# Kernel optimization log

Measured on AMD Instinct MI355X. Metric: run time of the kernel, lower is better.

Reference implementation:

```python
import jax, jax.numpy as jnp
import numpy as np

D_MODEL = 1024
D_FF = 4096
EPS = 1e-5


def layer_norm(x, gamma, beta):
    mu = jnp.mean(x, axis=-1, keepdims=True)
    var = jnp.var(x, axis=-1, keepdims=True)
    return (x - mu) * jax.lax.rsqrt(var + EPS) * gamma + beta


def attention(x_q, x_kv, WQ, WK, WV, causal):
    Q = x_q @ WQ          # [B,Sq,D]
    K = x_kv @ WK         # [B,Sk,D]
    V = x_kv @ WV
    scale = 1.0 / jnp.sqrt(jnp.asarray(Q.shape[-1], Q.dtype))
    scores = jnp.einsum('bqd,bkd->bqk', Q, K) * scale
    if causal:
        Sq, Sk = scores.shape[-2], scores.shape[-1]
        mask = jnp.triu(jnp.full((Sq, Sk), -jnp.inf, scores.dtype), k=1)
        scores = scores + mask
    attn = jax.nn.softmax(scores, axis=-1)
    return jnp.einsum('bqk,bkd->bqd', attn, V)


def setup_inputs() -> dict:
    key = jax.random.key(0)
    ks = jax.random.split(key, 16)
    B, S = 4, 2048
    s = 0.02
    inp = {
        'y': jax.random.normal(ks[0], (B, S, D_MODEL), jnp.float32),
        'Z': jax.random.normal(ks[1], (B, S, D_MODEL), jnp.float32),
        'WQ1': jax.random.normal(ks[2], (D_MODEL, D_MODEL), jnp.float32) * s,
        'WK1': jax.random.normal(ks[3], (D_MODEL, D_MODEL), jnp.float32) * s,
        'WV1': jax.random.normal(ks[4], (D_MODEL, D_MODEL), jnp.float32) * s,
        'WQ2': jax.random.normal(ks[5], (D_MODEL, D_MODEL), jnp.float32) * s,
        'WK2': jax.random.normal(ks[6], (D_MODEL, D_MODEL), jnp.float32) * s,
        'WV2': jax.random.normal(ks[7], (D_MODEL, D_MODEL), jnp.float32) * s,
        'W_ff1': jax.random.normal(ks[8], (D_MODEL, D_FF), jnp.float32) * s,
        'b_ff1': jnp.zeros((D_FF,), jnp.float32),
        'W_ff2': jax.random.normal(ks[9], (D_FF, D_MODEL), jnp.float32) * s,
        'b_ff2': jnp.zeros((D_MODEL,), jnp.float32),
        'g1': jnp.ones((D_MODEL,), jnp.float32), 'be1': jnp.zeros((D_MODEL,), jnp.float32),
        'g2': jnp.ones((D_MODEL,), jnp.float32), 'be2': jnp.zeros((D_MODEL,), jnp.float32),
        'g3': jnp.ones((D_MODEL,), jnp.float32), 'be3': jnp.zeros((D_MODEL,), jnp.float32),
    }
    return inp


def reference(y, Z, WQ1, WK1, WV1, WQ2, WK2, WV2, W_ff1, b_ff1, W_ff2, b_ff2,
              g1, be1, g2, be2, g3, be3):
    # masked self-attention + add&norm
    y = layer_norm(y + attention(y, y, WQ1, WK1, WV1, causal=True), g1, be1)
    # cross-attention + add&norm
    y = layer_norm(y + attention(y, Z, WQ2, WK2, WV2, causal=False), g2, be2)
    # FFN + add&norm
    h = jax.nn.relu(y @ W_ff1 + b_ff1) @ W_ff2 + b_ff2
    y = layer_norm(y + h, g3, be3)
    return y
```

## Files before the change

### kernel.cpp

```cpp
#include <hip/hip_runtime.h>
#include <cstddef>

typedef unsigned short u16;
typedef __attribute__((ext_vector_type(8))) short bf16x8;
typedef __attribute__((ext_vector_type(4))) float f32x4;

__device__ __forceinline__ u16 f2bf(float f) {
  union { float f; unsigned u; } x; x.f = f;
  unsigned r = x.u + 0x7fffu + ((x.u >> 16) & 1u);
  return (u16)(r >> 16);
}
__device__ __forceinline__ float bf2f(u16 h) {
  union { unsigned u; float f; } x; x.u = ((unsigned)h) << 16;
  return x.f;
}

__device__ __forceinline__ void gll16(const u16* g, u16* ldsbase) {
  __builtin_amdgcn_global_load_lds(
      (const __attribute__((address_space(1))) void*)g,
      (__attribute__((address_space(3))) void*)ldsbase, 16, 0, 0);
}

__global__ __launch_bounds__(256) void f32_to_bf16(const float* __restrict__ in,
                                                   u16* __restrict__ out, size_t n) {
  size_t i = (size_t)blockIdx.x * 256 + threadIdx.x;
  if (i < n) out[i] = f2bf(in[i]);
}

__global__ __launch_bounds__(256) void transpose_f32_bf16(const float* __restrict__ in,
                                                          u16* __restrict__ out,
                                                          int R, int C) {
  __shared__ float tile[32][33];
  int c0 = blockIdx.x * 32, r0 = blockIdx.y * 32;
  int tx = threadIdx.x & 31, ty = threadIdx.x >> 5;
  #pragma unroll
  for (int i = ty; i < 32; i += 8)
    tile[i][tx] = in[(size_t)(r0 + i) * C + c0 + tx];
  __syncthreads();
  #pragma unroll
  for (int i = ty; i < 32; i += 8)
    out[(size_t)(c0 + i) * R + r0 + tx] = f2bf(tile[tx][i]);
}

enum { EPI_F32 = 0, EPI_BF16 = 1, EPI_BF16_SCALE = 2,
       EPI_SPLIT = 3, EPI_BIAS_RELU_BF16 = 4, EPI_BIAS_F32 = 5 };

template <int EPI>
__global__ __launch_bounds__(256) void gemm_bt(
    const u16* __restrict__ A, const u16* __restrict__ Bt,
    void* __restrict__ C0, void* __restrict__ C1, const float* __restrict__ bias,
    int N, int K, int lda, int ldb, int ldc, int split,
    long long sA, long long sB, int sC)
{
  constexpr bool SW = (EPI != EPI_SPLIT);
  __shared__ __align__(16) u16 lA[2][128 * 32];
  __shared__ __align__(16) u16 lB[2][128 * 32];

  const unsigned gx = gridDim.x, gxy = gridDim.x * gridDim.y;
  unsigned id = blockIdx.x + gx * blockIdx.y + gxy * blockIdx.z;
  const unsigned nb = gxy * gridDim.z;
  unsigned p = id;
  if ((nb & 7u) == 0u) p = (id & 7u) * (nb >> 3) + (id >> 3);
  const int z  = p / gxy;
  const unsigned rem = p % gxy;
  const int m0 = (int)(rem / gx) * 128;
  const int n0 = (int)(rem % gx) * 128;

  A  += (long long)z * sA;
  Bt += (long long)z * sB;

  const int t    = threadIdx.x;
  const int lane = t & 63;
  const int wave = t >> 6;
  const int wm   = (wave >> 1) * 64;
  const int wn   = (wave & 1) * 64;
  const int quad = lane >> 4;
  const int lrow = lane & 15;

  const int srow = lane >> 2;
  const int scol = ((lane & 3) ^ ((srow >> 1) & 3)) * 8;
  const u16* gA = A  + (size_t)(m0 + wave * 16 + srow) * lda + scol;
  const u16* gB = Bt + (size_t)(n0 + wave * 16 + srow) * ldb + scol;
  const size_t a64 = (size_t)64 * lda, b64 = (size_t)64 * ldb;
  const int wo = wave * 512;

  const int pq = (quad ^ ((lrow >> 1) & 3)) * 8;

  f32x4 acc[4][4];
  const f32x4 zero = {0.f, 0.f, 0.f, 0.f};
  #pragma unroll
  for (int i = 0; i < 4; i++)
    #pragma unroll
    for (int j = 0; j < 4; j++) acc[i][j] = zero;

  gll16(gA, &lA[0][wo]);
  gll16(gA + a64, &lA[0][wo + 64 * 32]);
  gll16(gB, &lB[0][wo]);
  gll16(gB + b64, &lB[0][wo + 64 * 32]);

  int buf = 0;
  for (int k0 = 0; k0 < K; k0 += 32, buf ^= 1) {
    __syncthreads();
    if (k0 + 32 < K) {
      gll16(gA + k0 + 32, &lA[buf ^ 1][wo]);
      gll16(gA + a64 + k0 + 32, &lA[buf ^ 1][wo + 64 * 32]);
      gll16(gB + k0 + 32, &lB[buf ^ 1][wo]);
      gll16(gB + b64 + k0 + 32, &lB[buf ^ 1][wo + 64 * 32]);
    }

    bf16x8 af[4], bfr[4];
    #pragma unroll
    for (int mt = 0; mt < 4; mt++)
      af[mt] = *(const bf16x8*)(&lA[buf][(wm + mt * 16 + lrow) * 32 + pq]);
    #pragma unroll
    for (int nt = 0; nt < 4; nt++)
      bfr[nt] = *(const bf16x8*)(&lB[buf][(wn + nt * 16 + lrow) * 32 + pq]);

    #pragma unroll
    for (int mt = 0; mt < 4; mt++)
      #pragma unroll
      for (int nt = 0; nt < 4; nt++) {
        if constexpr (SW)
          acc[mt][nt] = __builtin_amdgcn_mfma_f32_16x16x32_bf16(bfr[nt], af[mt], acc[mt][nt], 0, 0, 0);
        else
          acc[mt][nt] = __builtin_amdgcn_mfma_f32_16x16x32_bf16(af[mt], bfr[nt], acc[mt][nt], 0, 0, 0);
      }
  }

  const unsigned zoff = (unsigned)z * (unsigned)sC;
  if constexpr (SW) {
    #pragma unroll
    for (int mt = 0; mt < 4; mt++) {
      #pragma unroll
      for (int nt = 0; nt < 4; nt++) {
        const unsigned m  = (unsigned)(m0 + wm + mt * 16 + lrow);
        const unsigned nc = (unsigned)(n0 + wn + nt * 16 + quad * 4);
        const unsigned idx = zoff + m * (unsigned)ldc + nc;
        f32x4 v = acc[mt][nt];
        if constexpr (EPI == EPI_F32) {
          *(float4*)((float*)C0 + idx) = make_float4(v[0], v[1], v[2], v[3]);
        } else if constexpr (EPI == EPI_BF16) {
          ushort4 o; o.x = f2bf(v[0]); o.y = f2bf(v[1]); o.z = f2bf(v[2]); o.w = f2bf(v[3]);
          *(ushort4*)((u16*)C0 + idx) = o;
        } else if constexpr (EPI == EPI_BF16_SCALE) {
          ushort4 o;
          o.x = f2bf(v[0] * 0.03125f); o.y = f2bf(v[1] * 0.03125f);
          o.z = f2bf(v[2] * 0.03125f); o.w = f2bf(v[3] * 0.03125f);
          *(ushort4*)((u16*)C0 + idx) = o;
        } else if constexpr (EPI == EPI_BIAS_RELU_BF16) {
          const float4 bb = *(const float4*)(bias + nc);
          float y0 = v[0] + bb.x, y1 = v[1] + bb.y, y2 = v[2] + bb.z, y3 = v[3] + bb.w;
          ushort4 o;
          o.x = f2bf(y0 > 0.f ? y0 : 0.f); o.y = f2bf(y1 > 0.f ? y1 : 0.f);
          o.z = f2bf(y2 > 0.f ? y2 : 0.f); o.w = f2bf(y3 > 0.f ? y3 : 0.f);
          *(ushort4*)((u16*)C0 + idx) = o;
        } else {
          const float4 bb = *(const float4*)(bias + nc);
          *(float4*)((float*)C0 + idx) =
              make_float4(v[0] + bb.x, v[1] + bb.y, v[2] + bb.z, v[3] + bb.w);
        }
      }
    }
  } else {
    #pragma unroll
    for (int mt = 0; mt < 4; mt++) {
      #pragma unroll
      for (int nt = 0; nt < 4; nt++) {
        const int row0 = m0 + wm + mt * 16 + quad * 4;
        const int col  = n0 + wn + nt * 16 + lrow;
        if (col < split) {
          const unsigned b0 = (unsigned)row0 * (unsigned)ldc + (unsigned)col;
          #pragma unroll
          for (int r = 0; r < 4; r++)
            ((u16*)C0)[b0 + (unsigned)r * ldc] = f2bf(acc[mt][nt][r]);
        } else {
          const int zp = row0 >> 11;
          const int s  = row0 & 2047;
          const unsigned vo = (unsigned)zp * (unsigned)sC
                            + (unsigned)(col - split) * 2048u + (unsigned)s;
          ushort4 o4;
          o4.x = f2bf(acc[mt][nt][0]); o4.y = f2bf(acc[mt][nt][1]);
          o4.z = f2bf(acc[mt][nt][2]); o4.w = f2bf(acc[mt][nt][3]);
          *(ushort4*)((u16*)C1 + vo) = o4;
        }
      }
    }
  }
}

__global__ __launch_bounds__(256) void softmax_bf16(u16* __restrict__ SP, int causal) {
  __shared__ float red[8];
  const int row = blockIdx.x;
  const int q = row & 2047;
  u16* p = SP + (size_t)row * 2048;
  const int t = threadIdx.x;
  const int base = t * 8;
  const int limit = causal ? (q + 1) : 2048;

  uint4 raw = *(const uint4*)(p + base);
  unsigned w[4] = {raw.x, raw.y, raw.z, raw.w};
  float v[8];
  #pragma unroll
  for (int j = 0; j < 4; j++) {
    union { unsigned u; float f; } lo, hi;
    lo.u = w[j] << 16; hi.u = w[j] & 0xffff0000u;
    v[2 * j] = lo.f; v[2 * j + 1] = hi.f;
  }
  #pragma unroll
  for (int j = 0; j < 8; j++) if (base + j >= limit) v[j] = -3.4e38f;

  float mx = v[0];
  #pragma unroll
  for (int j = 1; j < 8; j++) mx = fmaxf(mx, v[j]);
  #pragma unroll
  for (int o = 32; o > 0; o >>= 1) mx = fmaxf(mx, __shfl_down(mx, o));
  if ((t & 63) == 0) red[t >> 6] = mx;
  __syncthreads();
  mx = fmaxf(fmaxf(red[0], red[1]), fmaxf(red[2], red[3]));

  float s = 0.f;
  #pragma unroll
  for (int j = 0; j < 8; j++) { float e = __expf(v[j] - mx); v[j] = e; s += e; }
  #pragma unroll
  for (int o = 32; o > 0; o >>= 1) s += __shfl_down(s, o);
  if ((t & 63) == 0) red[4 + (t >> 6)] = s;
  __syncthreads();
  const float inv = 1.f / (red[4] + red[5] + red[6] + red[7]);

  unsigned o4[4];
  #pragma unroll
  for (int j = 0; j < 4; j++)
    o4[j] = (unsigned)f2bf(v[2 * j] * inv) | ((unsigned)f2bf(v[2 * j + 1] * inv) << 16);
  *(uint4*)(p + base) = make_uint4(o4[0], o4[1], o4[2], o4[3]);
}

template <int ABF>
__global__ __launch_bounds__(256) void ln_residual(const void* __restrict__ a_,
                                                   const float* __restrict__ b,
                                                   const float* __restrict__ g,
                                                   const float* __restrict__ be,
                                                   float* __restrict__ outf,
                                                   u16* __restrict__ outb) {
  __shared__ float red[8];
  const size_t base = (size_t)blockIdx.x * 1024;
  const int t = threadIdx.x;
  const int i0 = t * 4;

  float va[4];
  if constexpr (ABF) {
    const ushort4 h = *(const ushort4*)((const u16*)a_ + base + i0);
    va[0] = bf2f(h.x); va[1] = bf2f(h.y); va[2] = bf2f(h.z); va[3] = bf2f(h.w);
  } else {
    const float4 f = *(const float4*)((const float*)a_ + base + i0);
    va[0] = f.x; va[1] = f.y; va[2] = f.z; va[3] = f.w;
  }
  const float4 vb = *(const float4*)(b + base + i0);
  float v[4] = {va[0] + vb.x, va[1] + vb.y, va[2] + vb.z, va[3] + vb.w};

  float s = v[0] + v[1] + v[2] + v[3];
  #pragma unroll
  for (int o = 32; o > 0; o >>= 1) s += __shfl_down(s, o);
  if ((t & 63) == 0) red[t >> 6] = s;
  __syncthreads();
  const float mean = (red[0] + red[1] + red[2] + red[3]) * (1.f / 1024.f);

  float qq = 0.f;
  #pragma unroll
  for (int i = 0; i < 4; i++) { float d = v[i] - mean; qq += d * d; }
  #pragma unroll
  for (int o = 32; o > 0; o >>= 1) qq += __shfl_down(qq, o);
  if ((t & 63) == 0) red[4 + (t >> 6)] = qq;
  __syncthreads();
  const float rstd = rsqrtf((red[4] + red[5] + red[6] + red[7]) * (1.f / 1024.f) + 1e-5f);

  const float4 gg = *(const float4*)(g + i0);
  const float4 bb = *(const float4*)(be + i0);
  float y0 = (v[0] - mean) * rstd * gg.x + bb.x;
  float y1 = (v[1] - mean) * rstd * gg.y + bb.y;
  float y2 = (v[2] - mean) * rstd * gg.z + bb.z;
  float y3 = (v[3] - mean) * rstd * gg.w + bb.w;
  if (outf) *(float4*)(outf + base + i0) = make_float4(y0, y1, y2, y3);
  if (outb) {
    ushort4 o4; o4.x = f2bf(y0); o4.y = f2bf(y1); o4.z = f2bf(y2); o4.w = f2bf(y3);
    *(ushort4*)(outb + base + i0) = o4;
  }
}

extern "C" void kernel_launch(void* const* d_in, const int* in_sizes, int n_in,
                              void* d_out, int out_size, void* d_ws, size_t ws_size,
                              hipStream_t stream)
{
  const float* y_in = (const float*)d_in[0];
  const float* Z_in = (const float*)d_in[1];
  const float* WQ1  = (const float*)d_in[2];
  const float* WK1  = (const float*)d_in[3];
  const float* WV1  = (const float*)d_in[4];
  const float* WQ2  = (const float*)d_in[5];
  const float* WK2  = (const float*)d_in[6];
  const float* WV2  = (const float*)d_in[7];
  const float* Wff1 = (const float*)d_in[8];
  const float* bff1 = (const float*)d_in[9];
  const float* Wff2 = (const float*)d_in[10];
  const float* bff2 = (const float*)d_in[11];
  const float* g1  = (const float*)d_in[12];
  const float* be1 = (const float*)d_in[13];
  const float* g2  = (const float*)d_in[14];
  const float* be2 = (const float*)d_in[15];
  const float* g3  = (const float*)d_in[16];
  const float* be3 = (const float*)d_in[17];
  (void)in_sizes; (void)n_in; (void)out_size;

  constexpr int Bn = 4, S = 2048, D = 1024, DF = 4096;
  constexpr long long BS = (long long)Bn * S;
  const long long SD = (long long)S * D, SS = (long long)S * S, DS = (long long)D * S;

  char* ws = (char*)d_ws;
  size_t off = 0;
  auto alloc = [&](size_t bytes) -> char* {
    char* p = ws + off;
    off += (bytes + 255) & ~(size_t)255;
    return p;
  };

  u16* wq1t  = (u16*)alloc((size_t)D * D * 2);
  u16* wk1t  = (u16*)alloc((size_t)D * D * 2);
  u16* wv1t  = (u16*)alloc((size_t)D * D * 2);
  u16* wq2t  = (u16*)alloc((size_t)D * D * 2);
  u16* wk2t  = (u16*)alloc((size_t)D * D * 2);
  u16* wv2t  = (u16*)alloc((size_t)D * D * 2);
  u16* wff1t = (u16*)alloc((size_t)D * DF * 2);
  u16* wff2t = (u16*)alloc((size_t)D * DF * 2);
  u16* ybf   = (u16*)alloc((size_t)BS * D * 2);
  u16* zbf   = (u16*)alloc((size_t)BS * D * 2);
  u16* QKb   = (u16*)alloc((size_t)BS * 2 * D * 2);
  u16* Vtb   = (u16*)alloc((size_t)Bn * D * S * 2);
  u16* SPb   = (u16*)alloc((size_t)Bn * S * S * 2);
  float* attnF = (float*)alloc((size_t)BS * D * 4);
  u16*   y1b = ybf;
  u16*   y2b = zbf;
  u16*   Hb  = QKb;
  float* Fb  = attnF;

  if (off > ws_size) return;

  const dim3 blk(256);

  f32_to_bf16<<<dim3((unsigned)((BS * D) / 256)), blk, 0, stream>>>(y_in, ybf, (size_t)BS * D);
  f32_to_bf16<<<dim3((unsigned)((BS * D) / 256)), blk, 0, stream>>>(Z_in, zbf, (size_t)BS * D);
  transpose_f32_bf16<<<dim3(D / 32, D / 32), blk, 0, stream>>>(WQ1, wq1t, D, D);
  transpose_f32_bf16<<<dim3(D / 32, D / 32), blk, 0, stream>>>(WK1, wk1t, D, D);
  transpose_f32_bf16<<<dim3(D / 32, D / 32), blk, 0, stream>>>(WV1, wv1t, D, D);
  transpose_f32_bf16<<<dim3(D / 32, D / 32), blk, 0, stream>>>(WQ2, wq2t, D, D);
  transpose_f32_bf16<<<dim3(D / 32, D / 32), blk, 0, stream>>>(WK2, wk2t, D, D);
  transpose_f32_bf16<<<dim3(D / 32, D / 32), blk, 0, stream>>>(WV2, wv2t, D, D);
  transpose_f32_bf16<<<dim3(DF / 32, D / 32), blk, 0, stream>>>(Wff1, wff1t, D, DF);
  transpose_f32_bf16<<<dim3(D / 32, DF / 32), blk, 0, stream>>>(Wff2, wff2t, DF, D);

  gemm_bt<EPI_SPLIT><<<dim3(3 * D / 128, BS / 128, 1), blk, 0, stream>>>(
      ybf, wq1t, QKb, Vtb, nullptr, 3 * D, D, D, D, 2 * D, 2 * D, 0, 0, (int)DS);
  gemm_bt<EPI_BF16_SCALE><<<dim3(S / 128, S / 128, Bn), blk, 0, stream>>>(
      QKb, QKb + D, SPb, nullptr, nullptr, S, D, 2 * D, 2 * D, S, 0, SD * 2, SD * 2, (int)SS);
  softmax_bf16<<<dim3((unsigned)(Bn * S)), blk, 0, stream>>>(SPb, 1);
  gemm_bt<EPI_F32><<<dim3(D / 128, S / 128, Bn), blk, 0, stream>>>(
      SPb, Vtb, attnF, nullptr, nullptr, D, S, S, S, D, 0, SS, DS, (int)SD);
  ln_residual<0><<<dim3((unsigned)BS), blk, 0, stream>>>(y_in, attnF, g1, be1, nullptr, y1b);

  gemm_bt<EPI_BF16><<<dim3(D / 128, BS / 128, 1), blk, 0, stream>>>(
      y1b, wq2t, QKb, nullptr, nullptr, D, D, D, D, 2 * D, 0, 0, 0, 0);
  gemm_bt<EPI_SPLIT><<<dim3(2 * D / 128, BS / 128, 1), blk, 0, stream>>>(
      zbf, wk2t, QKb + D, Vtb, nullptr, 2 * D, D, D, D, 2 * D, D, 0, 0, (int)DS);
  gemm_bt<EPI_BF16_SCALE><<<dim3(S / 128, S / 128, Bn), blk, 0, stream>>>(
      QKb, QKb + D, SPb, nullptr, nullptr, S, D, 2 * D, 2 * D, S, 0, SD * 2, SD * 2, (int)SS);
  softmax_bf16<<<dim3((unsigned)(Bn * S)), blk, 0, stream>>>(SPb, 0);
  gemm_bt<EPI_F32><<<dim3(D / 128, S / 128, Bn), blk, 0, stream>>>(
      SPb, Vtb, attnF, nullptr, nullptr, D, S, S, S, D, 0, SS, DS, (int)SD);
  ln_residual<1><<<dim3((unsigned)BS), blk, 0, stream>>>(y1b, attnF, g2, be2, nullptr, y2b);

  gemm_bt<EPI_BIAS_RELU_BF16><<<dim3(DF / 128, BS / 128, 1), blk, 0, stream>>>(
      y2b, wff1t, Hb, nullptr, bff1, DF, D, D, D, DF, 0, 0, 0, 0);
  gemm_bt<EPI_BIAS_F32><<<dim3(D / 128, BS / 128, 1), blk, 0, stream>>>(
      Hb, wff2t, Fb, nullptr, bff2, D, DF, DF, DF, D, 0, 0, 0, 0);
  ln_residual<1><<<dim3((unsigned)BS), blk, 0, stream>>>(y2b, Fb, g3, be3, (float*)d_out, nullptr);
}
```

Baseline: 832.4 us.

## Replace 128x128 GEMM with 256x256 8-wave pipelined kernel and causal skipping

Replaces the 128x128x32 double-buffered GEMM with a 256x256x64 tile kernel using 512 threads. Each k-step is split into four phases that interleave LDS fragment loads, async global-to-LDS staging and MFMA bursts, with raised wave priority around the MFMAs. It also skips masked work in causal self-attention: the QK^T GEMM runs only on lower-triangular tiles, and the PV GEMM stops its K loop at the diagonal. V is now produced as a separate transposed GEMM instead of through the split epilogue. Larger tiles raise LDS use and register pressure and mean fewer blocks per GEMM, and the causal path relies on the softmax writing zeros into the unwritten upper-triangle region.

```diff
diff --git a/kernel.cpp b/kernel.cpp
--- a/kernel.cpp
+++ b/kernel.cpp
@@ -43,146 +43,229 @@
 }
 
 enum { EPI_F32 = 0, EPI_BF16 = 1, EPI_BF16_SCALE = 2,
-       EPI_SPLIT = 3, EPI_BIAS_RELU_BF16 = 4, EPI_BIAS_F32 = 5 };
-
-template <int EPI>
-__global__ __launch_bounds__(256) void gemm_bt(
+       EPI_BIAS_RELU_BF16 = 3, EPI_BIAS_F32 = 4 };
+enum { MODE_FULL = 0, MODE_TRI = 1, MODE_CAUSAL_K = 2 };
+
+template <int EPI, int MODE>
+__global__ __launch_bounds__(512) void gemm256(
     const u16* __restrict__ A, const u16* __restrict__ Bt,
-    void* __restrict__ C0, void* __restrict__ C1, const float* __restrict__ bias,
-    int N, int K, int lda, int ldb, int ldc, int split,
-    long long sA, long long sB, int sC)
+    void* __restrict__ C0, const float* __restrict__ bias,
+    int K, int lda, int ldb, int ldc,
+    long long sA, long long sB, long long sC)
 {
-  constexpr bool SW = (EPI != EPI_SPLIT);
-  __shared__ __align__(16) u16 lA[2][128 * 32];
-  __shared__ __align__(16) u16 lB[2][128 * 32];
+  __shared__ __align__(16) u16 lA[2][256 * 64];
+  __shared__ __align__(16) u16 lB[2][256 * 64];
 
   const unsigned gx = gridDim.x, gxy = gridDim.x * gridDim.y;
   unsigned id = blockIdx.x + gx * blockIdx.y + gxy * blockIdx.z;
   const unsigned nb = gxy * gridDim.z;
   unsigned p = id;
   if ((nb & 7u) == 0u) p = (id & 7u) * (nb >> 3) + (id >> 3);
-  const int z  = p / gxy;
-  const unsigned rem = p % gxy;
-  const int m0 = (int)(rem / gx) * 128;
-  const int n0 = (int)(rem % gx) * 128;
+  int z, mi, ni;
+  if constexpr (MODE == MODE_TRI) {
+    z = (int)(p / gxy);
+    int r = (int)(p % gxy);
+    int m = 0;
+    while ((m + 1) * (m + 2) / 2 <= r) m++;
+    mi = m; ni = r - m * (m + 1) / 2;
+  } else {
+    z = (int)(p / gxy);
+    const unsigned rem = p % gxy;
+    mi = (int)(rem / gx);
+    ni = (int)(rem % gx);
+  }
+  const int m0 = mi * 256, n0 = ni * 256;
 
   A  += (long long)z * sA;
   Bt += (long long)z * sB;
+
+  int NT = K >> 6;
+  if constexpr (MODE == MODE_CAUSAL_K) NT = (m0 + 256) >> 6;
 
   const int t    = threadIdx.x;
   const int lane = t & 63;
   const int wave = t >> 6;
-  const int wm   = (wave >> 1) * 64;
-  const int wn   = (wave & 1) * 64;
+  const int wr   = wave >> 2;
+  const int wc   = wave & 3;
   const int quad = lane >> 4;
   const int lrow = lane & 15;
 
-  const int srow = lane >> 2;
-  const int scol = ((lane & 3) ^ ((srow >> 1) & 3)) * 8;
-  const u16* gA = A  + (size_t)(m0 + wave * 16 + srow) * lda + scol;
-  const u16* gB = Bt + (size_t)(n0 + wave * 16 + srow) * ldb + scol;
+  const int srow = lane >> 3;
+  const int scol = ((lane & 7) ^ srow) * 8;
+  const u16* gAp = A  + (size_t)(m0 + wave * 8 + srow) * lda + scol;
+  const u16* gBp = Bt + (size_t)(n0 + wave * 8 + srow) * ldb + scol;
   const size_t a64 = (size_t)64 * lda, b64 = (size_t)64 * ldb;
-  const int wo = wave * 512;
-
-  const int pq = (quad ^ ((lrow >> 1) & 3)) * 8;
-
-  f32x4 acc[4][4];
+  const int lw = wave * 512;
+
+  const int pg0 = (quad ^ (lrow & 7)) * 8;
+  const int pg1 = pg0 ^ 32;
+  const int rA = (wr * 128 + lrow) * 64;
+  const int rB = (wc * 64 + lrow) * 64;
+
+  f32x4 acc[8][4];
   const f32x4 zero = {0.f, 0.f, 0.f, 0.f};
   #pragma unroll
-  for (int i = 0; i < 4; i++)
+  for (int i = 0; i < 8; i++)
     #pragma unroll
     for (int j = 0; j < 4; j++) acc[i][j] = zero;
 
-  gll16(gA, &lA[0][wo]);
-  gll16(gA + a64, &lA[0][wo + 64 * 32]);
-  gll16(gB, &lB[0][wo]);
-  gll16(gB + b64, &lB[0][wo + 64 * 32]);
-
-  int buf = 0;
-  for (int k0 = 0; k0 < K; k0 += 32, buf ^= 1) {
-    __syncthreads();
-    if (k0 + 32 < K) {
-      gll16(gA + k0 + 32, &lA[buf ^ 1][wo]);
-      gll16(gA + a64 + k0 + 32, &lA[buf ^ 1][wo + 64 * 32]);
-      gll16(gB + k0 + 32, &lB[buf ^ 1][wo]);
-      gll16(gB + b64 + k0 + 32, &lB[buf ^ 1][wo + 64 * 32]);
-    }
-
-    bf16x8 af[4], bfr[4];
-    #pragma unroll
-    for (int mt = 0; mt < 4; mt++)
-      af[mt] = *(const bf16x8*)(&lA[buf][(wm + mt * 16 + lrow) * 32 + pq]);
-    #pragma unroll
-    for (int nt = 0; nt < 4; nt++)
-      bfr[nt] = *(const bf16x8*)(&lB[buf][(wn + nt * 16 + lrow) * 32 + pq]);
-
-    #pragma unroll
-    for (int mt = 0; mt < 4; mt++)
-      #pragma unroll
-      for (int nt = 0; nt < 4; nt++) {
-        if constexpr (SW)
-          acc[mt][nt] = __builtin_amdgcn_mfma_f32_16x16x32_bf16(bfr[nt], af[mt], acc[mt][nt], 0, 0, 0);
-        else
-          acc[mt][nt] = __builtin_amdgcn_mfma_f32_16x16x32_bf16(af[mt], bfr[nt], acc[mt][nt], 0, 0, 0);
-      }
-  }
-
-  const unsigned zoff = (unsigned)z * (unsigned)sC;
-  if constexpr (SW) {
-    #pragma unroll
-    for (int mt = 0; mt < 4; mt++) {
-      #pragma unroll
-      for (int nt = 0; nt < 4; nt++) {
-        const unsigned m  = (unsigned)(m0 + wm + mt * 16 + lrow);
-        const unsigned nc = (unsigned)(n0 + wn + nt * 16 + quad * 4);
-        const unsigned idx = zoff + m * (unsigned)ldc + nc;
-        f32x4 v = acc[mt][nt];
-        if constexpr (EPI == EPI_F32) {
-          *(float4*)((float*)C0 + idx) = make_float4(v[0], v[1], v[2], v[3]);
-        } else if constexpr (EPI == EPI_BF16) {
-          ushort4 o; o.x = f2bf(v[0]); o.y = f2bf(v[1]); o.z = f2bf(v[2]); o.w = f2bf(v[3]);
-          *(ushort4*)((u16*)C0 + idx) = o;
-        } else if constexpr (EPI == EPI_BF16_SCALE) {
-          ushort4 o;
-          o.x = f2bf(v[0] * 0.03125f); o.y = f2bf(v[1] * 0.03125f);
-          o.z = f2bf(v[2] * 0.03125f); o.w = f2bf(v[3] * 0.03125f);
-          *(ushort4*)((u16*)C0 + idx) = o;
-        } else if constexpr (EPI == EPI_BIAS_RELU_BF16) {
-          const float4 bb = *(const float4*)(bias + nc);
-          float y0 = v[0] + bb.x, y1 = v[1] + bb.y, y2 = v[2] + bb.z, y3 = v[3] + bb.w;
-          ushort4 o;
-          o.x = f2bf(y0 > 0.f ? y0 : 0.f); o.y = f2bf(y1 > 0.f ? y1 : 0.f);
-          o.z = f2bf(y2 > 0.f ? y2 : 0.f); o.w = f2bf(y3 > 0.f ? y3 : 0.f);
-          *(ushort4*)((u16*)C0 + idx) = o;
-        } else {
-          const float4 bb = *(const float4*)(bias + nc);
-          *(float4*)((float*)C0 + idx) =
-              make_float4(v[0] + bb.x, v[1] + bb.y, v[2] + bb.z, v[3] + bb.w);
-        }
-      }
-    }
+  auto stage = [&](int b, int s, int kt) {
+    const int k = kt * 64;
+    if (s == 0) {
+      gll16(gBp + k,            &lB[b][lw]);
+      gll16(gBp + k + b64,      &lB[b][4096 + lw]);
+    } else if (s == 1) {
+      gll16(gBp + k + 2 * b64,  &lB[b][8192 + lw]);
+      gll16(gBp + k + 3 * b64,  &lB[b][12288 + lw]);
+    } else if (s == 2) {
+      gll16(gAp + k,            &lA[b][lw]);
+      gll16(gAp + k + a64,      &lA[b][4096 + lw]);
+    } else {
+      gll16(gAp + k + 2 * a64,  &lA[b][8192 + lw]);
+      gll16(gAp + k + 3 * a64,  &lA[b][12288 + lw]);
+    }
+  };
+
+  stage(0, 0, 0); stage(0, 1, 0); stage(0, 2, 0); stage(0, 3, 0);
+  if (NT > 1) {
+    stage(1, 0, 1); stage(1, 1, 1); stage(1, 2, 1);
+    asm volatile("s_waitcnt vmcnt(6)" ::: "memory");
   } else {
-    #pragma unroll
-    for (int mt = 0; mt < 4; mt++) {
-      #pragma unroll
-      for (int nt = 0; nt < 4; nt++) {
-        const int row0 = m0 + wm + mt * 16 + quad * 4;
-        const int col  = n0 + wn + nt * 16 + lrow;
-        if (col < split) {
-          const unsigned b0 = (unsigned)row0 * (unsigned)ldc + (unsigned)col;
-          #pragma unroll
-          for (int r = 0; r < 4; r++)
-            ((u16*)C0)[b0 + (unsigned)r * ldc] = f2bf(acc[mt][nt][r]);
-        } else {
-          const int zp = row0 >> 11;
-          const int s  = row0 & 2047;
-          const unsigned vo = (unsigned)zp * (unsigned)sC
-                            + (unsigned)(col - split) * 2048u + (unsigned)s;
-          ushort4 o4;
-          o4.x = f2bf(acc[mt][nt][0]); o4.y = f2bf(acc[mt][nt][1]);
-          o4.z = f2bf(acc[mt][nt][2]); o4.w = f2bf(acc[mt][nt][3]);
-          *(ushort4*)((u16*)C1 + vo) = o4;
-        }
+    asm volatile("s_waitcnt vmcnt(0)" ::: "memory");
+  }
+  __builtin_amdgcn_s_barrier();
+
+  bf16x8 af[4][2], bfr[4][2];
+
+  for (int kt = 0; kt < NT; ++kt) {
+    const int bsel = kt & 1;
+    const u16* sa = &lA[bsel][0];
+    const u16* sb = &lB[bsel][0];
+
+    #pragma unroll
+    for (int mf = 0; mf < 4; ++mf) {
+      af[mf][0] = *(const bf16x8*)(sa + rA + mf * 1024 + pg0);
+      af[mf][1] = *(const bf16x8*)(sa + rA + mf * 1024 + pg1);
+    }
+    if (wc < 2) {
+      #pragma unroll
+      for (int nf = 0; nf < 4; ++nf) {
+        bfr[nf][0] = *(const bf16x8*)(sb + rB + nf * 1024 + pg0);
+        bfr[nf][1] = *(const bf16x8*)(sb + rB + nf * 1024 + pg1);
+      }
+    } else {
+      #pragma unroll
+      for (int nf = 0; nf < 2; ++nf) {
+        bfr[nf][0] = *(const bf16x8*)(sb + rB + nf * 1024 + pg0);
+        bfr[nf][1] = *(const bf16x8*)(sb + rB + nf * 1024 + pg1);
+      }
+    }
+    if (kt + 1 < NT) stage(bsel ^ 1, 3, kt + 1);
+    __builtin_amdgcn_s_barrier();
+    asm volatile("s_waitcnt lgkmcnt(0)" ::: "memory");
+    __builtin_amdgcn_sched_barrier(0);
+    __builtin_amdgcn_s_setprio(1);
+    #pragma unroll
+    for (int mf = 0; mf < 4; ++mf)
+      #pragma unroll
+      for (int nf = 0; nf < 2; ++nf) {
+        acc[mf][nf] = __builtin_amdgcn_mfma_f32_16x16x32_bf16(bfr[nf][0], af[mf][0], acc[mf][nf], 0, 0, 0);
+        acc[mf][nf] = __builtin_amdgcn_mfma_f32_16x16x32_bf16(bfr[nf][1], af[mf][1], acc[mf][nf], 0, 0, 0);
+      }
+    __builtin_amdgcn_s_setprio(0);
+    __builtin_amdgcn_s_barrier();
+
+    if (wc >= 2) {
+      #pragma unroll
+      for (int nf = 2; nf < 4; ++nf) {
+        bfr[nf][0] = *(const bf16x8*)(sb + rB + nf * 1024 + pg0);
+        bfr[nf][1] = *(const bf16x8*)(sb + rB + nf * 1024 + pg1);
+      }
+    }
+    if (kt + 2 < NT) stage(bsel, 0, kt + 2);
+    __builtin_amdgcn_s_barrier();
+    asm volatile("s_waitcnt lgkmcnt(0)" ::: "memory");
+    __builtin_amdgcn_sched_barrier(0);
+    __builtin_amdgcn_s_setprio(1);
+    #pragma unroll
+    for (int mf = 0; mf < 4; ++mf)
+      #pragma unroll
+      for (int nf = 2; nf < 4; ++nf) {
+        acc[mf][nf] = __builtin_amdgcn_mfma_f32_16x16x32_bf16(bfr[nf][0], af[mf][0], acc[mf][nf], 0, 0, 0);
+        acc[mf][nf] = __builtin_amdgcn_mfma_f32_16x16x32_bf16(bfr[nf][1], af[mf][1], acc[mf][nf], 0, 0, 0);
+      }
+    __builtin_amdgcn_s_setprio(0);
+    __builtin_amdgcn_s_barrier();
+
+    #pragma unroll
+    for (int mf = 0; mf < 4; ++mf) {
+      af[mf][0] = *(const bf16x8*)(sa + rA + (mf + 4) * 1024 + pg0);
+      af[mf][1] = *(const bf16x8*)(sa + rA + (mf + 4) * 1024 + pg1);
+    }
+    if (kt + 2 < NT) stage(bsel, 1, kt + 2);
+    __builtin_amdgcn_s_barrier();
+    asm volatile("s_waitcnt lgkmcnt(0)" ::: "memory");
+    __builtin_amdgcn_sched_barrier(0);
+    __builtin_amdgcn_s_setprio(1);
+    #pragma unroll
+    for (int mf = 0; mf < 4; ++mf)
+      #pragma unroll
+      for (int nf = 2; nf < 4; ++nf) {
+        acc[mf + 4][nf] = __builtin_amdgcn_mfma_f32_16x16x32_bf16(bfr[nf][0], af[mf][0], acc[mf + 4][nf], 0, 0, 0);
+        acc[mf + 4][nf] = __builtin_amdgcn_mfma_f32_16x16x32_bf16(bfr[nf][1], af[mf][1], acc[mf + 4][nf], 0, 0, 0);
+      }
+    __builtin_amdgcn_s_setprio(0);
+    __builtin_amdgcn_s_barrier();
+
+    if (kt + 2 < NT) {
+      stage(bsel, 2, kt + 2);
+      asm volatile("s_waitcnt vmcnt(6)" ::: "memory");
+    } else if (kt + 1 < NT) {
+      asm volatile("s_waitcnt vmcnt(0)" ::: "memory");
+    }
+    __builtin_amdgcn_s_barrier();
+    __builtin_amdgcn_s_setprio(1);
+    #pragma unroll
+    for (int mf = 0; mf < 4; ++mf)
+      #pragma unroll
+      for (int nf = 0; nf < 2; ++nf) {
+        acc[mf + 4][nf] = __builtin_amdgcn_mfma_f32_16x16x32_bf16(bfr[nf][0], af[mf][0], acc[mf + 4][nf], 0, 0, 0);
+        acc[mf + 4][nf] = __builtin_amdgcn_mfma_f32_16x16x32_bf16(bfr[nf][1], af[mf][1], acc[mf + 4][nf], 0, 0, 0);
+      }
+    __builtin_amdgcn_s_setprio(0);
+    __builtin_amdgcn_s_barrier();
+  }
+
+  const size_t zoff = (size_t)((long long)z * sC);
+  #pragma unroll
+  for (int mf = 0; mf < 8; ++mf) {
+    #pragma unroll
+    for (int nf = 0; nf < 4; ++nf) {
+      const size_t m  = (size_t)(m0 + wr * 128 + mf * 16 + lrow);
+      const size_t nc = (size_t)(n0 + wc * 64 + nf * 16 + quad * 4);
+      const size_t idx = zoff + m * (size_t)ldc + nc;
+      f32x4 v = acc[mf][nf];
+      if constexpr (EPI == EPI_F32) {
+        *(float4*)((float*)C0 + idx) = make_float4(v[0], v[1], v[2], v[3]);
+      } else if constexpr (EPI == EPI_BF16) {
+        ushort4 o; o.x = f2bf(v[0]); o.y = f2bf(v[1]); o.z = f2bf(v[2]); o.w = f2bf(v[3]);
+        *(ushort4*)((u16*)C0 + idx) = o;
+      } else if constexpr (EPI == EPI_BF16_SCALE) {
+        ushort4 o;
+        o.x = f2bf(v[0] * 0.03125f); o.y = f2bf(v[1] * 0.03125f);
+        o.z = f2bf(v[2] * 0.03125f); o.w = f2bf(v[3] * 0.03125f);
+        *(ushort4*)((u16*)C0 + idx) = o;
+      } else if constexpr (EPI == EPI_BIAS_RELU_BF16) {
+        const float4 bb = *(const float4*)(bias + nc);
+        float y0 = v[0] + bb.x, y1 = v[1] + bb.y, y2 = v[2] + bb.z, y3 = v[3] + bb.w;
+        ushort4 o;
+        o.x = f2bf(y0 > 0.f ? y0 : 0.f); o.y = f2bf(y1 > 0.f ? y1 : 0.f);
+        o.z = f2bf(y2 > 0.f ? y2 : 0.f); o.w = f2bf(y3 > 0.f ? y3 : 0.f);
+        *(ushort4*)((u16*)C0 + idx) = o;
+      } else {
+        const float4 bb = *(const float4*)(bias + nc);
+        *(float4*)((float*)C0 + idx) =
+            make_float4(v[0] + bb.x, v[1] + bb.y, v[2] + bb.z, v[3] + bb.w);
       }
     }
   }
@@ -312,7 +395,9 @@
 
   constexpr int Bn = 4, S = 2048, D = 1024, DF = 4096;
   constexpr long long BS = (long long)Bn * S;
-  const long long SD = (long long)S * D, SS = (long long)S * S, DS = (long long)D * S;
+  const long long SD = (long long)S * D;
+  const long long SS = (long long)S * S;
+  const long long SD2 = (long long)S * 2 * D;
 
   char* ws = (char*)d_ws;
   size_t off = 0;
@@ -333,7 +418,7 @@
   u16* ybf   = (u16*)alloc((size_t)BS * D * 2);
   u16* zbf   = (u16*)alloc((size_t)BS * D * 2);
   u16* QKb   = (u16*)alloc((size_t)BS * 2 * D * 2);
-  u16* Vtb   = (u16*)alloc((size_t)Bn * D * S * 2);
+  u16* Vtb   = (u16*)alloc((size_t)D * BS * 2);
   u16* SPb   = (u16*)alloc((size_t)Bn * S * S * 2);
   float* attnF = (float*)alloc((size_t)BS * D * 4);
   u16*   y1b = ybf;
@@ -344,6 +429,7 @@
   if (off > ws_size) return;
 
   const dim3 blk(256);
+  const dim3 blk512(512);
 
   f32_to_bf16<<<dim3((unsigned)((BS * D) / 256)), blk, 0, stream>>>(y_in, ybf, (size_t)BS * D);
   f32_to_bf16<<<dim3((unsigned)((BS * D) / 256)), blk, 0, stream>>>(Z_in, zbf, (size_t)BS * D);
@@ -356,29 +442,33 @@
   transpose_f32_bf16<<<dim3(DF / 32, D / 32), blk, 0, stream>>>(Wff1, wff1t, D, DF);
   transpose_f32_bf16<<<dim3(D / 32, DF / 32), blk, 0, stream>>>(Wff2, wff2t, DF, D);
 
-  gemm_bt<EPI_SPLIT><<<dim3(3 * D / 128, BS / 128, 1), blk, 0, stream>>>(
-      ybf, wq1t, QKb, Vtb, nullptr, 3 * D, D, D, D, 2 * D, 2 * D, 0, 0, (int)DS);
-  gemm_bt<EPI_BF16_SCALE><<<dim3(S / 128, S / 128, Bn), blk, 0, stream>>>(
-      QKb, QKb + D, SPb, nullptr, nullptr, S, D, 2 * D, 2 * D, S, 0, SD * 2, SD * 2, (int)SS);
+  gemm256<EPI_BF16, MODE_FULL><<<dim3(2 * D / 256, BS / 256, 1), blk512, 0, stream>>>(
+      ybf, wq1t, QKb, nullptr, D, D, D, 2 * D, 0, 0, 0);
+  gemm256<EPI_BF16, MODE_FULL><<<dim3((unsigned)(BS / 256), D / 256, 1), blk512, 0, stream>>>(
+      wv1t, ybf, Vtb, nullptr, D, D, D, (int)BS, 0, 0, 0);
+  gemm256<EPI_BF16_SCALE, MODE_TRI><<<dim3(36, 1, Bn), blk512, 0, stream>>>(
+      QKb, QKb + D, SPb, nullptr, D, 2 * D, 2 * D, S, SD2, SD2, SS);
   softmax_bf16<<<dim3((unsigned)(Bn * S)), blk, 0, stream>>>(SPb, 1);
-  gemm_bt<EPI_F32><<<dim3(D / 128, S / 128, Bn), blk, 0, stream>>>(
-      SPb, Vtb, attnF, nullptr, nullptr, D, S, S, S, D, 0, SS, DS, (int)SD);
+  gemm256<EPI_F32, MODE_CAUSAL_K><<<dim3(D / 256, S / 256, Bn), blk512, 0, stream>>>(
+      SPb, Vtb, attnF, nullptr, S, S, (int)BS, D, SS, S, SD);
   ln_residual<0><<<dim3((unsigned)BS), blk, 0, stream>>>(y_in, attnF, g1, be1, nullptr, y1b);
 
-  gemm_bt<EPI_BF16><<<dim3(D / 128, BS / 128, 1), blk, 0, stream>>>(
-      y1b, wq2t, QKb, nullptr, nullptr, D, D, D, D, 2 * D, 0, 0, 0, 0);
-  gemm_bt<EPI_SPLIT><<<dim3(2 * D / 128, BS / 128, 1), blk, 0, stream>>>(
-      zbf, wk2t, QKb + D, Vtb, nullptr, 2 * D, D, D, D, 2 * D, D, 0, 0, (int)DS);
-  gemm_bt<EPI_BF16_SCALE><<<dim3(S / 128, S / 128, Bn), blk, 0, stream>>>(
-      QKb, QKb + D, SPb, nullptr, nullptr, S, D, 2 * D, 2 * D, S, 0, SD * 2, SD * 2, (int)SS);
+  gemm256<EPI_BF16, MODE_FULL><<<dim3(D / 256, BS / 256, 1), blk512, 0, stream>>>(
+      y1b, wq2t, QKb, nullptr, D, D, D, 2 * D, 0, 0, 0);
+  gemm256<EPI_BF16, MODE_FULL><<<dim3(D / 256, BS / 256, 1), blk512, 0, stream>>>(
+      zbf, wk2t, QKb + D, nullptr, D, D, D, 2 * D, 0, 0, 0);
+  gemm256<EPI_BF16, MODE_FULL><<<dim3((unsigned)(BS / 256), D / 256, 1), blk512, 0, stream>>>(
+      wv2t, zbf, Vtb, nullptr, D, D, D, (int)BS, 0, 0, 0);
+  gemm256<EPI_BF16_SCALE, MODE_FULL><<<dim3(S / 256, S / 256, Bn), blk512, 0, stream>>>(
+      QKb, QKb + D, SPb, nullptr, D, 2 * D, 2 * D, S, SD2, SD2, SS);
   softmax_bf16<<<dim3((unsigned)(Bn * S)), blk, 0, stream>>>(SPb, 0);
-  gemm_bt<EPI_F32><<<dim3(D / 128, S / 128, Bn), blk, 0, stream>>>(
-      SPb, Vtb, attnF, nullptr, nullptr, D, S, S, S, D, 0, SS, DS, (int)SD);
+  gemm256<EPI_F32, MODE_FULL><<<dim3(D / 256, S / 256, Bn), blk512, 0, stream>>>(
+      SPb, Vtb, attnF, nullptr, S, S, (int)BS, D, SS, S, SD);
   ln_residual<1><<<dim3((unsigned)BS), blk, 0, stream>>>(y1b, attnF, g2, be2, nullptr, y2b);
 
-  gemm_bt<EPI_BIAS_RELU_BF16><<<dim3(DF / 128, BS / 128, 1), blk, 0, stream>>>(
-      y2b, wff1t, Hb, nullptr, bff1, DF, D, D, D, DF, 0, 0, 0, 0);
-  gemm_bt<EPI_BIAS_F32><<<dim3(D / 128, BS / 128, 1), blk, 0, stream>>>(
-      Hb, wff2t, Fb, nullptr, bff2, D, DF, DF, DF, D, 0, 0, 0, 0);
+  gemm256<EPI_BIAS_RELU_BF16, MODE_FULL><<<dim3(DF / 256, BS / 256, 1), blk512, 0, stream>>>(
+      y2b, wff1t, Hb, bff1, D, D, D, DF, 0, 0, 0);
+  gemm256<EPI_BIAS_F32, MODE_FULL><<<dim3(D / 256, BS / 256, 1), blk512, 0, stream>>>(
+      Hb, wff2t, Fb, bff2, DF, DF, DF, D, 0, 0, 0);
   ln_residual<1><<<dim3((unsigned)BS), blk, 0, stream>>>(y2b, Fb, g3, be3, (float*)d_out, nullptr);
 }
```

Result: slower. 870.7 us (+4.6%).
